# Optimization experiments

Measured on AMD Instinct MI355X. Metric: run time of the kernel, lower is better.

The kernel has to match this reference:

```python
import jax, jax.numpy as jnp
import numpy as np

N, INC, INN, OUTC, OUTN, MAXD = 16, 32, 65536, 32, 8192, 16

def setup_inputs() -> dict:
    key = jax.random.key(0)
    ks = jax.random.split(key, 7)
    x = jax.random.normal(ks[0], (N, INC, INN), jnp.float32)
    A = jax.random.randint(ks[1], (OUTN, MAXD), 0, INN, dtype=jnp.int64)
    weight = 0.2 * jax.random.normal(ks[2], (INC, INN), jnp.float32)
    # normalize=True with fixed degree MAXD -> mask = 1/maxD everywhere
    mask = jnp.ones((OUTN, MAXD, 1), jnp.float32) / MAXD
    mask_weight = 0.2 * jax.random.normal(ks[3], (OUTN, MAXD, 1), jnp.float32)
    ct_weight = jax.random.normal(ks[4], (OUTC, INC), jnp.float32) / np.sqrt(INC)
    ct_bias = 0.02 * jax.random.normal(ks[5], (OUTC,), jnp.float32)
    bias = 0.2 * jax.random.normal(ks[6], (OUTC, OUTN), jnp.float32)
    return {"x": x, "A": A, "weight": weight, "mask": mask,
            "mask_weight": mask_weight, "ct_weight": ct_weight,
            "ct_bias": ct_bias, "bias": bias}

def reference(x, A, weight, mask, mask_weight, ct_weight, ct_bias, bias):
    n, inc, inn = x.shape
    outn, maxD = A.shape
    # per-input-node channel scaling, then lay out as (inn, N*inc) feature table
    feat = (x * weight).reshape(n * inc, inn).T            # (inn, N*inc)
    emb = feat[A]                                          # (outn, maxD, N*inc) gather
    w = mask_weight * mask                                 # (outn, maxD, 1)
    pooled = (w * emb).reshape(outn, maxD, n, inc).sum(axis=1)  # (outn, N, inc)
    almost_y = jnp.einsum('onc,dc->ond', pooled, ct_weight) + ct_bias  # (outn, N, outc)
    return almost_y.transpose(1, 2, 0) + bias              # (N, outc, outn)
```

## Files before the change

### kernel.cpp

```cpp
#include <hip/hip_runtime.h>
#include <hip/hip_bf16.h>

#define NN    16
#define INC   32
#define INN   65536
#define OUTC  32
#define OUTN  8192
#define MAXD  16
#define NC    512

typedef __attribute__((ext_vector_type(8))) unsigned short ushort8;

__global__ __launch_bounds__(256) void transpose_scale_kernel(
    const float* __restrict__ x,
    const float* __restrict__ weight,
    unsigned short* __restrict__ feat)
{
    __shared__ float tile[64][65];
    const int l  = threadIdx.x;
    const int j0 = blockIdx.x * 64;
    const int r0 = blockIdx.y * 64;

    #pragma unroll
    for (int it = 0; it < 4; ++it) {
        int idx = it * 256 + l;
        int rl  = idx >> 4;
        int jj  = idx & 15;
        int r   = r0 + rl;
        int c   = r & 31;
        int j   = j0 + jj * 4;
        float4 xv = *reinterpret_cast<const float4*>(x + (size_t)r * INN + j);
        float4 wv = *reinterpret_cast<const float4*>(weight + (size_t)c * INN + j);
        tile[jj * 4 + 0][rl] = xv.x * wv.x;
        tile[jj * 4 + 1][rl] = xv.y * wv.y;
        tile[jj * 4 + 2][rl] = xv.z * wv.z;
        tile[jj * 4 + 3][rl] = xv.w * wv.w;
    }
    __syncthreads();

    #pragma unroll
    for (int p = 0; p < 2; ++p) {
        int jl = p * 32 + (l >> 3);
        int rs = (l & 7) * 8;
        ushort8 pk;
        #pragma unroll
        for (int k = 0; k < 8; ++k) {
            float v = tile[jl][rs + k];
            pk[k] = __bfloat16_as_ushort(__float2bfloat16(v));
        }
        *reinterpret_cast<ushort8*>(
            feat + (size_t)(j0 + jl) * NC + r0 + rs) = pk;
    }
}

#define OTILE 16

__global__ __launch_bounds__(256) void gather_gemm_kernel(
    const unsigned short* __restrict__ feat,
    const int*   __restrict__ A,
    const float* __restrict__ mask,
    const float* __restrict__ mw,
    const float* __restrict__ ctw,
    const float* __restrict__ ctb,
    const float* __restrict__ bias,
    float*       __restrict__ out)
{
    __shared__ float pooled[OTILE][NC];
    const int l    = threadIdx.x;
    const int wave = l >> 6;
    const int lane = l & 63;
    const int o0   = blockIdx.x * OTILE;

    const int dout = l & 31;
    float ctr[32];
    #pragma unroll
    for (int q = 0; q < 8; ++q)
        *reinterpret_cast<float4*>(&ctr[4 * q]) =
            *reinterpret_cast<const float4*>(ctw + dout * 32 + 4 * q);
    const float cb = ctb[dout];

    #pragma unroll
    for (int i = 0; i < 4; ++i) {
        const int o  = wave * 4 + i;
        const int oo = o0 + o;
        float acc[8] = {0.f, 0.f, 0.f, 0.f, 0.f, 0.f, 0.f, 0.f};
        #pragma unroll
        for (int d = 0; d < MAXD; ++d) {
            int   j = A[oo * MAXD + d] & (INN - 1);
            float w = mw[oo * MAXD + d] * mask[oo * MAXD + d];
            ushort8 p = *reinterpret_cast<const ushort8*>(
                feat + (size_t)j * NC + lane * 8);
            #pragma unroll
            for (int k = 0; k < 8; ++k)
                acc[k] += w * __uint_as_float((unsigned)p[k] << 16);
        }
        *reinterpret_cast<float4*>(&pooled[o][lane * 8]) =
            make_float4(acc[0], acc[1], acc[2], acc[3]);
        *reinterpret_cast<float4*>(&pooled[o][lane * 8 + 4]) =
            make_float4(acc[4], acc[5], acc[6], acc[7]);
    }
    __syncthreads();

    #pragma unroll
    for (int h = 0; h < 2; ++h) {
        const int n = (l >> 5) + 8 * h;
        float vals[OTILE];
        #pragma unroll
        for (int o = 0; o < OTILE; ++o) {
            float s = cb;
            #pragma unroll
            for (int q = 0; q < 8; ++q) {
                float4 pv = *reinterpret_cast<const float4*>(
                    &pooled[o][n * 32 + 4 * q]);
                s += pv.x * ctr[4 * q + 0] + pv.y * ctr[4 * q + 1]
                   + pv.z * ctr[4 * q + 2] + pv.w * ctr[4 * q + 3];
            }
            vals[o] = s + bias[(size_t)dout * OUTN + o0 + o];
        }
        float4* outp = reinterpret_cast<float4*>(
            out + ((size_t)(n * 32 + dout)) * OUTN + o0);
        #pragma unroll
        for (int q = 0; q < 4; ++q)
            outp[q] = make_float4(vals[4*q], vals[4*q+1], vals[4*q+2], vals[4*q+3]);
    }
}

extern "C" void kernel_launch(void* const* d_in, const int* in_sizes, int n_in,
                              void* d_out, int out_size, void* d_ws, size_t ws_size,
                              hipStream_t stream)
{
    const float* x      = (const float*)d_in[0];
    const int*   A      = (const int*)  d_in[1];
    const float* weight = (const float*)d_in[2];
    const float* mask   = (const float*)d_in[3];
    const float* mw     = (const float*)d_in[4];
    const float* ctw    = (const float*)d_in[5];
    const float* ctb    = (const float*)d_in[6];
    const float* bias   = (const float*)d_in[7];
    float* out = (float*)d_out;

    unsigned short* feat = (unsigned short*)d_ws;

    dim3 gA(INN / 64, NC / 64);
    transpose_scale_kernel<<<gA, 256, 0, stream>>>(x, weight, feat);

    gather_gemm_kernel<<<OUTN / OTILE, 256, 0, stream>>>(
        feat, A, mask, mw, ctw, ctb, bias, out);
}
```

Before: 258.3 us.

## Remap channel-mix epilogue so each thread computes two outputs per pooled load

The epilogue mapping changes so each thread owns one sample n and two output channels (d0, d0+16). Each pooled float4 read from shared memory now feeds two dot products, where before every thread read its own copy. The shared-memory index is rotated by n to spread bank accesses. Bias is loaded as float4 vectors before the loop, and the ct_weight load moves after the gather phase. The cost is about 32 more registers per thread for the second weight row, which could lower occupancy.

```diff
diff --git a/kernel.cpp b/kernel.cpp
--- a/kernel.cpp
+++ b/kernel.cpp
@@ -71,13 +71,8 @@
     const int lane = l & 63;
     const int o0   = blockIdx.x * OTILE;
 
-    const int dout = l & 31;
-    float ctr[32];
-    #pragma unroll
-    for (int q = 0; q < 8; ++q)
-        *reinterpret_cast<float4*>(&ctr[4 * q]) =
-            *reinterpret_cast<const float4*>(ctw + dout * 32 + 4 * q);
-    const float cb = ctb[dout];
+    const int n  = l >> 4;
+    const int d0 = l & 15;
 
     #pragma unroll
     for (int i = 0; i < 4; ++i) {
@@ -99,29 +94,58 @@
         *reinterpret_cast<float4*>(&pooled[o][lane * 8 + 4]) =
             make_float4(acc[4], acc[5], acc[6], acc[7]);
     }
+
+    float ctr0[32], ctr1[32];
+    #pragma unroll
+    for (int q = 0; q < 8; ++q) {
+        const int qq = (q + n) & 7;
+        *reinterpret_cast<float4*>(&ctr0[4 * q]) =
+            *reinterpret_cast<const float4*>(ctw + d0 * 32 + 4 * qq);
+        *reinterpret_cast<float4*>(&ctr1[4 * q]) =
+            *reinterpret_cast<const float4*>(ctw + (d0 + 16) * 32 + 4 * qq);
+    }
+    const float cb0 = ctb[d0];
+    const float cb1 = ctb[d0 + 16];
+
     __syncthreads();
 
+    float4 b0[4], b1[4];
     #pragma unroll
-    for (int h = 0; h < 2; ++h) {
-        const int n = (l >> 5) + 8 * h;
-        float vals[OTILE];
+    for (int q = 0; q < 4; ++q) {
+        b0[q] = *reinterpret_cast<const float4*>(
+            bias + (size_t)d0 * OUTN + o0 + 4 * q);
+        b1[q] = *reinterpret_cast<const float4*>(
+            bias + (size_t)(d0 + 16) * OUTN + o0 + 4 * q);
+    }
+
+    float v0[OTILE], v1[OTILE];
+    #pragma unroll
+    for (int o = 0; o < OTILE; ++o) {
+        const float* po = &pooled[o][n * 32];
+        float s0 = cb0, s1 = cb1;
         #pragma unroll
-        for (int o = 0; o < OTILE; ++o) {
-            float s = cb;
-            #pragma unroll
-            for (int q = 0; q < 8; ++q) {
-                float4 pv = *reinterpret_cast<const float4*>(
-                    &pooled[o][n * 32 + 4 * q]);
-                s += pv.x * ctr[4 * q + 0] + pv.y * ctr[4 * q + 1]
-                   + pv.z * ctr[4 * q + 2] + pv.w * ctr[4 * q + 3];
-            }
-            vals[o] = s + bias[(size_t)dout * OUTN + o0 + o];
+        for (int q = 0; q < 8; ++q) {
+            const int qq = (q + n) & 7;
+            float4 pv = *reinterpret_cast<const float4*>(po + 4 * qq);
+            s0 += pv.x * ctr0[4*q+0] + pv.y * ctr0[4*q+1]
+                + pv.z * ctr0[4*q+2] + pv.w * ctr0[4*q+3];
+            s1 += pv.x * ctr1[4*q+0] + pv.y * ctr1[4*q+1]
+                + pv.z * ctr1[4*q+2] + pv.w * ctr1[4*q+3];
         }
-        float4* outp = reinterpret_cast<float4*>(
-            out + ((size_t)(n * 32 + dout)) * OUTN + o0);
-        #pragma unroll
-        for (int q = 0; q < 4; ++q)
-            outp[q] = make_float4(vals[4*q], vals[4*q+1], vals[4*q+2], vals[4*q+3]);
+        v0[o] = s0;
+        v1[o] = s1;
+    }
+
+    float* r0p = out + (size_t)(n * 32 + d0)      * OUTN + o0;
+    float* r1p = out + (size_t)(n * 32 + d0 + 16) * OUTN + o0;
+    #pragma unroll
+    for (int q = 0; q < 4; ++q) {
+        *reinterpret_cast<float4*>(r0p + 4 * q) = make_float4(
+            v0[4*q+0] + b0[q].x, v0[4*q+1] + b0[q].y,
+            v0[4*q+2] + b0[q].z, v0[4*q+3] + b0[q].w);
+        *reinterpret_cast<float4*>(r1p + 4 * q) = make_float4(
+            v1[4*q+0] + b1[q].x, v1[4*q+1] + b1[q].y,
+            v1[4*q+2] + b1[q].z, v1[4*q+3] + b1[q].w);
     }
 }
 
```

Result: slower. 269.9 us (+4.5%).
